# Kernel tuning notes

Hardware: AMD Instinct MI355X
Metric: run time of the kernel (lower is better)

The kernel has to match this reference:

```python
import jax, jax.numpy as jnp
import numpy as np

BS, C_IN, NP, NA = 2, 64, 1024, 60
NA_OUT, KS, ANN = 60, 3, 8
C_OUT = 128


def setup_inputs() -> dict:
    key = jax.random.key(0)
    k1, k2, k3, k4 = jax.random.split(key, 4)
    feats = jax.random.normal(k1, (BS, C_IN, NP, NA), dtype=jnp.float32)
    # precomputed anchor-neighbor weights, normalized over the ann axis
    w = jax.random.uniform(k2, (NA_OUT, KS, ANN), dtype=jnp.float32)
    intra_w = w / jnp.sum(w, axis=-1, keepdims=True)
    intra_idx = jax.random.randint(k3, (NA_OUT, KS, ANN), 0, NA)
    # xavier-normal-ish weight for the basic conv, flattened [C_OUT, C_IN*KS]
    W = jax.random.normal(k4, (C_OUT, C_IN * KS), dtype=jnp.float32) * (2.0 / np.sqrt(C_IN * KS + C_OUT))
    bias = jnp.full((1, C_OUT, 1), 0.001, dtype=jnp.float32)
    return {"feats": feats, "intra_w": intra_w, "W": W, "bias": bias, "intra_idx": intra_idx}


def reference(feats, intra_w, W, bias, intra_idx):
    bs, c, npts, na = feats.shape
    na_out, ks, ann = intra_idx.shape
    dim_out = W.shape[0]
    # intra_zpconv_grouping_naive: gather over anchor axis then weighted sum over ann
    g = feats[:, :, :, intra_idx]                      # [b, c, p, o, k, a]
    grouped = jnp.einsum('bcpoka,oka->bckpo', g, intra_w)  # [b, c, ks, p, na_out]
    # BasicZPConv: view to [b, c*ks, p*na_out], W @ x + bias
    x = grouped.reshape(bs, c * ks, npts * na_out)
    out = jnp.einsum('oi,bin->bon', W, x) + bias       # [b, dim_out, p*na_out]
    return out.reshape(bs, dim_out, npts, na_out)
```

## Files before the change

kernel.cpp:

```cpp
#include <hip/hip_runtime.h>

#define NPTS 1024
#define NA   60
#define CIN  64
#define KSZ  3
#define ANN  8
#define COUT 128
#define KD   192

using bf16x8 = __attribute__((ext_vector_type(8))) short;
using f32x4  = __attribute__((ext_vector_type(4))) float;

__device__ __forceinline__ unsigned short f2bf(float f) {
    unsigned int u = __builtin_bit_cast(unsigned int, f);
    u += 0x7FFFu + ((u >> 16) & 1u);
    return (unsigned short)(u >> 16);
}

__global__ void build_tables(const float* __restrict__ intra_w,
                             const float* __restrict__ W,
                             const int*   __restrict__ intra_idx,
                             unsigned short* __restrict__ ws) {
    int f = blockIdx.x * 256 + threadIdx.x;
    if (f < 24576) {
        int j = f & 7, l = (f >> 3) & 63, x = f >> 9;
        int kt = x % 6, mt = x / 6;
        int m  = mt * 16 + (l & 15);
        int ip = kt * 32 + 8 * (l >> 4) + j;
        int c  = ip & 63, ks = ip >> 6;
        ws[f] = f2bf(W[m * KD + c * KSZ + ks]);
    } else if (f < 36864) {
        int f2 = f - 24576;
        int j = f2 & 7, l = (f2 >> 3) & 63;
        int kt = (f2 >> 9) & 1, nt = f2 >> 10;
        int np = nt * 16 + (l & 15);
        int ap = kt * 32 + 8 * (l >> 4) + j;
        float s = 0.f;
        if (np < 180 && ap < 60) {
            int ks = (np >= 120) ? 2 : ((np >= 60) ? 1 : 0);
            int o  = np - 60 * ks;
            const int*   ix = intra_idx + (o * KSZ + ks) * ANN;
            const float* wx = intra_w   + (o * KSZ + ks) * ANN;
            #pragma unroll
            for (int a = 0; a < ANN; a++) s += (ix[a] == ap) ? wx[a] : 0.f;
        }
        ws[f] = f2bf(s);
    }
}

__global__ __launch_bounds__(256, 4)
void intrazp_mfma(const float* __restrict__ feats,
                  const float* __restrict__ bias,
                  const unsigned short* __restrict__ ws,
                  float* __restrict__ out) {
    __shared__ __align__(16) unsigned short AsT[64 * 192];

    const int t    = threadIdx.x;
    const int wave = t >> 6, lane = t & 63;
    const int l15  = lane & 15, g = lane >> 4;
    const int bp   = blockIdx.x;
    const int b    = bp >> 10, p = bp & 1023;

    #pragma unroll
    for (int r = 0; r < 3; r++) AsT[60 * 192 + r * 256 + t] = 0;

    const unsigned short* Sfrag = ws + 24576;
    const int wm = wave & 1, wn = wave >> 1;

    bf16x8 bfr[12];
    #pragma unroll
    for (int i = 0; i < 12; i++)
        bfr[i] = *(const bf16x8*)(Sfrag + ((wn * 12 + i) * 64 + lane) * 8);

    bf16x8 a1[2][2];
    {
        const float* fb = feats + ((size_t)b * CIN * NPTS + p) * NA;
        #pragma unroll
        for (int mi = 0; mi < 2; mi++) {
            int c = (2 * wm + mi) * 16 + l15;
            const float* fr = fb + (size_t)c * NPTS * NA;
            #pragma unroll
            for (int kt = 0; kt < 2; kt++) {
                int a0 = kt * 32 + 8 * g;
                float4 lo = *(const float4*)(fr + a0);
                int ah = a0 + 4;
                float4 hi = *(const float4*)(fr + ((ah < NA) ? ah : 0));
                bf16x8 v;
                v[0] = (short)f2bf(lo.x); v[1] = (short)f2bf(lo.y);
                v[2] = (short)f2bf(lo.z); v[3] = (short)f2bf(lo.w);
                v[4] = (short)f2bf(hi.x); v[5] = (short)f2bf(hi.y);
                v[6] = (short)f2bf(hi.z); v[7] = (short)f2bf(hi.w);
                a1[mi][kt] = v;
            }
        }
    }

    #pragma unroll
    for (int ni = 0; ni < 6; ni++) {
        int nt = wn * 6 + ni;
        int np = nt * 16 + l15;
        int ks = (np >= 120) ? 2 : ((np >= 60) ? 1 : 0);
        int o  = np - 60 * ks;
        int sw = (o & 7) << 4;
        int rowbyte = o * 384;

        #pragma unroll
        for (int mi = 0; mi < 2; mi++) {
            f32x4 acc = {0.f, 0.f, 0.f, 0.f};
            acc = __builtin_amdgcn_mfma_f32_16x16x32_bf16(a1[mi][0], bfr[ni * 2 + 0], acc, 0, 0, 0);
            acc = __builtin_amdgcn_mfma_f32_16x16x32_bf16(a1[mi][1], bfr[ni * 2 + 1], acc, 0, 0, 0);
            if (np < 180) {
                int cbase = (2 * wm + mi) * 16 + 4 * g;
                int ipb   = ks * 64 + cbase;
                unsigned int lo = (unsigned int)f2bf(acc[0]) | ((unsigned int)f2bf(acc[1]) << 16);
                unsigned int hi = (unsigned int)f2bf(acc[2]) | ((unsigned int)f2bf(acc[3]) << 16);
                int byte = (rowbyte + ipb * 2) ^ sw;
                *(uint2*)((char*)AsT + byte) = make_uint2(lo, hi);
            }
        }
    }

    bf16x8 a2[2][6];
    #pragma unroll
    for (int mi = 0; mi < 2; mi++)
        #pragma unroll
        for (int kt = 0; kt < 6; kt++)
            a2[mi][kt] = *(const bf16x8*)(ws + (((wave * 2 + mi) * 6 + kt) * 64 + lane) * 8);

    __syncthreads();

    int rb[4], swz[4], ov[4];
    #pragma unroll
    for (int nt = 0; nt < 4; nt++) {
        int o = nt * 16 + l15;
        ov[nt]  = o;
        rb[nt]  = o * 384;
        swz[nt] = (o & 7) << 4;
    }

    f32x4 acc[2][4];
    #pragma unroll
    for (int mi = 0; mi < 2; mi++)
        #pragma unroll
        for (int nt = 0; nt < 4; nt++) acc[mi][nt] = (f32x4){0.f, 0.f, 0.f, 0.f};

    #pragma unroll
    for (int kt = 0; kt < 6; kt++) {
        int x = (kt * 32 + 8 * g) * 2;
        bf16x8 bb[4];
        #pragma unroll
        for (int nt = 0; nt < 4; nt++)
            bb[nt] = *(const bf16x8*)((char*)AsT + ((rb[nt] + x) ^ swz[nt]));
        #pragma unroll
        for (int mi = 0; mi < 2; mi++)
            #pragma unroll
            for (int nt = 0; nt < 4; nt++)
                acc[mi][nt] = __builtin_amdgcn_mfma_f32_16x16x32_bf16(a2[mi][kt], bb[nt], acc[mi][nt], 0, 0, 0);
    }

    #pragma unroll
    for (int mi = 0; mi < 2; mi++) {
        int cbase = (wave * 2 + mi) * 16 + 4 * g;
        float bv0 = bias[cbase + 0], bv1 = bias[cbase + 1];
        float bv2 = bias[cbase + 2], bv3 = bias[cbase + 3];
        float* ob = out + (((size_t)b * COUT + cbase) * NPTS + p) * NA;
        const size_t cs = (size_t)NPTS * NA;
        #pragma unroll
        for (int nt = 0; nt < 4; nt++) {
            if (ov[nt] < NA) {
                ob[0 * cs + ov[nt]] = acc[mi][nt][0] + bv0;
                ob[1 * cs + ov[nt]] = acc[mi][nt][1] + bv1;
                ob[2 * cs + ov[nt]] = acc[mi][nt][2] + bv2;
                ob[3 * cs + ov[nt]] = acc[mi][nt][3] + bv3;
            }
        }
    }
}

extern "C" void kernel_launch(void* const* d_in, const int* in_sizes, int n_in,
                              void* d_out, int out_size, void* d_ws, size_t ws_size,
                              hipStream_t stream) {
    const float* feats     = (const float*)d_in[0];
    const float* intra_w   = (const float*)d_in[1];
    const float* W         = (const float*)d_in[2];
    const float* bias      = (const float*)d_in[3];
    const int*   intra_idx = (const int*)d_in[4];
    float* out = (float*)d_out;
    unsigned short* ws = (unsigned short*)d_ws;

    build_tables<<<dim3(144), dim3(256), 0, stream>>>(intra_w, W, intra_idx, ws);
    intrazp_mfma<<<dim3(2 * NPTS), dim3(256), 0, stream>>>(feats, bias, ws, out);
}
```

Measured before the change: 122.1 us.

## Stage feats through LDS with coalesced loads and remap block order

Each block now cooperatively loads its 64x60 feature slice with contiguous float4 reads, converts it to bf16, and stores it into a swizzled LDS tile. The MFMA A fragments are then read from LDS rather than through strided per-lane global loads. Block IDs are also permuted so that consecutive blocks touch points 256 apart. The selection-matrix fragments are loaded per iteration instead of being held in twelve registers, which lowers register pressure. In exchange the kernel adds an extra barrier and 8 KB of LDS per block, which could reduce occupancy.

```diff
diff --git a/kernel.cpp b/kernel.cpp
--- a/kernel.cpp
+++ b/kernel.cpp
@@ -53,51 +53,60 @@
                   const float* __restrict__ bias,
                   const unsigned short* __restrict__ ws,
                   float* __restrict__ out) {
+    __shared__ __align__(16) unsigned short fsS[64 * 64];
     __shared__ __align__(16) unsigned short AsT[64 * 192];
 
     const int t    = threadIdx.x;
     const int wave = t >> 6, lane = t & 63;
     const int l15  = lane & 15, g = lane >> 4;
-    const int bp   = blockIdx.x;
-    const int b    = bp >> 10, p = bp & 1023;
-
-    #pragma unroll
-    for (int r = 0; r < 3; r++) AsT[60 * 192 + r * 256 + t] = 0;
+    const int bid = blockIdx.x;
+    const int bp  = (bid & 7) * 256 + (bid >> 3);
+    const int b   = bp >> 10, p = bp & 1023;
+
+    {
+        const float* fb = feats + (size_t)b * CIN * NPTS * NA + (size_t)p * NA;
+        #pragma unroll
+        for (int r = 0; r < 4; r++) {
+            int q = t + r * 256;
+            if (q < 960) {
+                int c = q / 15, w = q - c * 15;
+                float4 v = *(const float4*)(fb + (size_t)c * NPTS * NA + w * 4);
+                unsigned int lo = (unsigned int)f2bf(v.x) | ((unsigned int)f2bf(v.y) << 16);
+                unsigned int hi = (unsigned int)f2bf(v.z) | ((unsigned int)f2bf(v.w) << 16);
+                int byte = (c * 128 + w * 8) ^ ((c & 7) << 4);
+                *(uint2*)((char*)fsS + byte) = make_uint2(lo, hi);
+            }
+        }
+        if (t < 64) {
+            int byte = (t * 128 + 120) ^ ((t & 7) << 4);
+            *(uint2*)((char*)fsS + byte) = make_uint2(0u, 0u);
+        }
+        if (t < 192) {
+            *(uint2*)((char*)AsT + 60 * 384 + t * 8) = make_uint2(0u, 0u);
+        }
+    }
+    __syncthreads();
 
     const unsigned short* Sfrag = ws + 24576;
     const int wm = wave & 1, wn = wave >> 1;
 
-    bf16x8 bfr[12];
-    #pragma unroll
-    for (int i = 0; i < 12; i++)
-        bfr[i] = *(const bf16x8*)(Sfrag + ((wn * 12 + i) * 64 + lane) * 8);
-
     bf16x8 a1[2][2];
-    {
-        const float* fb = feats + ((size_t)b * CIN * NPTS + p) * NA;
-        #pragma unroll
-        for (int mi = 0; mi < 2; mi++) {
-            int c = (2 * wm + mi) * 16 + l15;
-            const float* fr = fb + (size_t)c * NPTS * NA;
-            #pragma unroll
-            for (int kt = 0; kt < 2; kt++) {
-                int a0 = kt * 32 + 8 * g;
-                float4 lo = *(const float4*)(fr + a0);
-                int ah = a0 + 4;
-                float4 hi = *(const float4*)(fr + ((ah < NA) ? ah : 0));
-                bf16x8 v;
-                v[0] = (short)f2bf(lo.x); v[1] = (short)f2bf(lo.y);
-                v[2] = (short)f2bf(lo.z); v[3] = (short)f2bf(lo.w);
-                v[4] = (short)f2bf(hi.x); v[5] = (short)f2bf(hi.y);
-                v[6] = (short)f2bf(hi.z); v[7] = (short)f2bf(hi.w);
-                a1[mi][kt] = v;
-            }
+    #pragma unroll
+    for (int mi = 0; mi < 2; mi++) {
+        int c = (2 * wm + mi) * 16 + l15;
+        #pragma unroll
+        for (int kt = 0; kt < 2; kt++) {
+            int byte = (c * 128 + kt * 64 + g * 16) ^ ((c & 7) << 4);
+            a1[mi][kt] = *(const bf16x8*)((char*)fsS + byte);
         }
     }
 
     #pragma unroll
     for (int ni = 0; ni < 6; ni++) {
         int nt = wn * 6 + ni;
+        bf16x8 b0 = *(const bf16x8*)(Sfrag + ((nt * 2 + 0) * 64 + lane) * 8);
+        bf16x8 b1 = *(const bf16x8*)(Sfrag + ((nt * 2 + 1) * 64 + lane) * 8);
+
         int np = nt * 16 + l15;
         int ks = (np >= 120) ? 2 : ((np >= 60) ? 1 : 0);
         int o  = np - 60 * ks;
@@ -107,8 +116,8 @@
         #pragma unroll
         for (int mi = 0; mi < 2; mi++) {
             f32x4 acc = {0.f, 0.f, 0.f, 0.f};
-            acc = __builtin_amdgcn_mfma_f32_16x16x32_bf16(a1[mi][0], bfr[ni * 2 + 0], acc, 0, 0, 0);
-            acc = __builtin_amdgcn_mfma_f32_16x16x32_bf16(a1[mi][1], bfr[ni * 2 + 1], acc, 0, 0, 0);
+            acc = __builtin_amdgcn_mfma_f32_16x16x32_bf16(a1[mi][0], b0, acc, 0, 0, 0);
+            acc = __builtin_amdgcn_mfma_f32_16x16x32_bf16(a1[mi][1], b1, acc, 0, 0, 0);
             if (np < 180) {
                 int cbase = (2 * wm + mi) * 16 + 4 * g;
                 int ipb   = ks * 64 + cbase;
```

Result: faster. 117.9 us (-3.4%).
